# Optimization experiments

Measured on AMD Instinct MI355X. Metric: run time of the kernel, lower is better.

The kernel has to match this reference:

```python
import jax, jax.numpy as jnp
import numpy as np

B, L, E, H, C, V = 2048, 64, 200, 128, 128, 50000
EPS = 1e-5

def _gru_dir(x, Wih, Whh, bih, bhh):
    # x: [B, L, E] -> [B, L, H]; torch GRU gate order (r, z, n)
    xp = jnp.einsum('ble,ge->blg', x, Wih) + bih  # [B, L, 3H]
    xp = jnp.transpose(xp, (1, 0, 2))             # [L, B, 3H]
    h0 = jnp.zeros((x.shape[0], Whh.shape[1]), x.dtype)
    def step(h, xt):
        hp = h @ Whh.T + bhh
        xr, xz, xn = jnp.split(xt, 3, axis=-1)
        hr, hz, hn = jnp.split(hp, 3, axis=-1)
        r = jax.nn.sigmoid(xr + hr)
        z = jax.nn.sigmoid(xz + hz)
        n = jnp.tanh(xn + r * hn)
        h_new = (1.0 - z) * n + z * h
        return h_new, h_new
    _, ys = jax.lax.scan(step, h0, xp)
    return jnp.transpose(ys, (1, 0, 2))

def setup_inputs():
    key = jax.random.key(0)
    ks = jax.random.split(key, 16)
    sh = 1.0 / float(np.sqrt(H))
    sp = 1.0 / float(np.sqrt(2 * H))
    u = lambda k, s, a: jax.random.uniform(k, s, jnp.float32, -a, a)
    return {
        'x': jax.random.randint(ks[0], (B, L), 0, V),
        'word_hidden_stat': jnp.zeros((2, B, H), jnp.float32),
        'sequence_lens': jax.random.randint(ks[1], (B,), 1, L + 1),
        'emb': jax.random.normal(ks[2], (V, E), jnp.float32),
        'Wih_f': u(ks[3], (3 * H, E), sh), 'Whh_f': u(ks[4], (3 * H, H), sh),
        'bih_f': u(ks[5], (3 * H,), sh), 'bhh_f': u(ks[6], (3 * H,), sh),
        'Wih_b': u(ks[7], (3 * H, E), sh), 'Whh_b': u(ks[8], (3 * H, H), sh),
        'bih_b': u(ks[9], (3 * H,), sh), 'bhh_b': u(ks[10], (3 * H,), sh),
        'Wp': u(ks[11], (C, 2 * H), sp), 'bp': u(ks[12], (C,), sp),
        'gamma': jnp.ones((L,), jnp.float32), 'beta': jnp.zeros((L,), jnp.float32),
        'ctx': jax.random.uniform(ks[13], (C,), jnp.float32, -0.1, 0.1),
    }

def reference(x, word_hidden_stat, sequence_lens, emb, Wih_f, Whh_f, bih_f, bhh_f,
              Wih_b, Whh_b, bih_b, bhh_b, Wp, bp, gamma, beta, ctx):
    we = emb[x]                                            # [B, L, E]
    out_f = _gru_dir(we, Wih_f, Whh_f, bih_f, bhh_f)
    out_b = _gru_dir(we[:, ::-1], Wih_b, Whh_b, bih_b, bhh_b)[:, ::-1]
    out = jnp.concatenate([out_f, out_b], axis=-1)          # [B, L, 2H]
    # vectorized equivalent of get_mask + _fetch: zero positions >= length
    mask = (jnp.arange(L)[None, :] < sequence_lens[:, None]).astype(out.dtype)
    out = out * mask[:, :, None]
    proj = jnp.einsum('bld,cd->blc', out, Wp) + bp          # [B, L, C]
    # BatchNorm1d(num_features=L) in training mode: normalize each seq position over (batch, C)
    mean = proj.mean(axis=(0, 2), keepdims=True)
    var = proj.var(axis=(0, 2), keepdims=True)
    proj = (proj - mean) * jax.lax.rsqrt(var + EPS)
    proj = proj * gamma[None, :, None] + beta[None, :, None]
    proj = jax.nn.relu(proj)
    att = jax.nn.softmax(proj @ ctx, axis=1)                # [B, L]
    return jnp.einsum('bld,bl->bd', out, att)               # [B, 2H]
```

## Files before the change

### kernel.cpp

```cpp
#include <hip/hip_runtime.h>
#include <math.h>

#define BB 2048
#define LL 64
#define EE 200
#define HH 128
#define CDIM 128
#define VV 50000
#define G3 384
#define PEW 768
#define D2H 256
#define EPSV 1e-5f

typedef __attribute__((ext_vector_type(8))) short short8v;
typedef __attribute__((ext_vector_type(4))) float f32x4;

__device__ __forceinline__ float fast_sigmoid(float v) {
    return __builtin_amdgcn_rcpf(1.f + __expf(-v));
}
__device__ __forceinline__ float fast_tanh(float a) {
    float e = __expf(-2.f * fabsf(a));
    float m = (1.f - e) * __builtin_amdgcn_rcpf(1.f + e);
    return copysignf(m, a);
}

__device__ __forceinline__ float bf2f(unsigned short u) {
    union { unsigned int i; float f; } c; c.i = ((unsigned int)u) << 16; return c.f;
}
__device__ __forceinline__ unsigned short f2bf(float f) {
    union { float f; unsigned int i; } c; c.f = f;
    unsigned int r = c.i + 0x7FFF + ((c.i >> 16) & 1);
    return (unsigned short)(r >> 16);
}
__device__ __forceinline__ float ldc(const float* p) { return *p; }
__device__ __forceinline__ float ldc(const unsigned short* p) { return bf2f(*p); }
__device__ __forceinline__ void stc(float* p, float v) { *p = v; }
__device__ __forceinline__ void stc(unsigned short* p, float v) { *p = f2bf(v); }
__device__ __forceinline__ float4 ld4(const float* p) { return *(const float4*)p; }
__device__ __forceinline__ float4 ld4(const unsigned short* p) {
    ushort4 u = *(const ushort4*)p;
    return make_float4(bf2f(u.x), bf2f(u.y), bf2f(u.z), bf2f(u.w));
}

__global__ void zero_stats_kernel(float* __restrict__ stats) {
    if (threadIdx.x < 2 * LL) stats[threadIdx.x] = 0.f;
}

template <typename T>
__global__ __launch_bounds__(256) void pe_kernel(
    const float* __restrict__ emb,
    const float* __restrict__ Wih_f, const float* __restrict__ bih_f,
    const float* __restrict__ Wih_b, const float* __restrict__ bih_b,
    T* __restrict__ PE)
{
    __shared__ float As[8][136];
    __shared__ float Bs[8][136];
    const int mb = blockIdx.x * 128;
    const int nb = blockIdx.y * 128;
    const float* W  = (nb < G3) ? Wih_f : Wih_b;
    const float* bi = (nb < G3) ? bih_f : bih_b;
    const int nloc  = (nb < G3) ? nb : nb - G3;
    const int t  = threadIdx.x;
    const int tr = t >> 4, tc = t & 15;
    const int r  = t >> 1, q = t & 1;
    float acc[8][8] = {};
    for (int k0 = 0; k0 < EE; k0 += 8) {
        float4 av, bv;
        const int arow = mb + r;
        if (arow < VV) av = *(const float4*)(emb + (size_t)arow * EE + k0 + q * 4);
        else           av = make_float4(0.f, 0.f, 0.f, 0.f);
        bv = *(const float4*)(W + (size_t)(nloc + r) * EE + k0 + q * 4);
        __syncthreads();
        #pragma unroll
        for (int m = 0; m < 4; ++m) {
            As[q * 4 + m][r] = (&av.x)[m];
            Bs[q * 4 + m][r] = (&bv.x)[m];
        }
        __syncthreads();
        #pragma unroll
        for (int k = 0; k < 8; ++k) {
            float4 a0 = *(const float4*)&As[k][tr * 4];
            float4 a1 = *(const float4*)&As[k][64 + tr * 4];
            float4 b0 = *(const float4*)&Bs[k][tc * 4];
            float4 b1 = *(const float4*)&Bs[k][64 + tc * 4];
            float a8[8] = {a0.x,a0.y,a0.z,a0.w,a1.x,a1.y,a1.z,a1.w};
            float b8[8] = {b0.x,b0.y,b0.z,b0.w,b1.x,b1.y,b1.z,b1.w};
            #pragma unroll
            for (int i = 0; i < 8; ++i)
                #pragma unroll
                for (int j = 0; j < 8; ++j)
                    acc[i][j] = fmaf(a8[i], b8[j], acc[i][j]);
        }
    }
    #pragma unroll
    for (int i = 0; i < 8; ++i) {
        const int rl  = (i < 4) ? (tr * 4 + i) : (64 + tr * 4 + i - 4);
        const int row = mb + rl;
        if (row >= VV) continue;
        #pragma unroll
        for (int j = 0; j < 8; ++j) {
            const int cl = (j < 4) ? (tc * 4 + j) : (64 + tc * 4 + j - 4);
            stc(&PE[(size_t)row * PEW + nb + cl], acc[i][j] + bi[nloc + cl]);
        }
    }
}

__global__ void transpose4_kernel(const float* __restrict__ src,
                                  float* __restrict__ dst, int R, int K) {
    int idx = blockIdx.x * blockDim.x + threadIdx.x;
    int total = R * (K >> 2);
    if (idx >= total) return;
    int k4 = idx / R, r = idx - k4 * R;
    float4 v;
    v.x = src[r * K + k4 * 4 + 0];
    v.y = src[r * K + k4 * 4 + 1];
    v.z = src[r * K + k4 * 4 + 2];
    v.w = src[r * K + k4 * 4 + 3];
    ((float4*)dst)[idx] = v;
}

__global__ __launch_bounds__(64) void pack_whh_kernel(
    const float* __restrict__ Whh_f, const float* __restrict__ Whh_b,
    unsigned short* __restrict__ Wpk)
{
    const int fid = blockIdx.x;
    const int l   = threadIdx.x;
    const int g   = fid % 3;
    const int kt  = (fid / 3) & 3;
    const int p   = (fid / 12) & 1;
    const int w   = (fid / 24) & 7;
    const int dir = fid / 192;
    const float* W = dir ? Whh_b : Whh_f;
    const int n  = g * HH + w * 16 + (l & 15);
    const int k0 = kt * 32 + (l >> 4) * 8;
    unsigned short* dst = Wpk + (size_t)fid * 512 + l * 8;
    #pragma unroll
    for (int r = 0; r < 8; ++r) {
        float v = W[(size_t)n * HH + k0 + r];
        unsigned short hi = f2bf(v);
        dst[r] = p ? f2bf(v - bf2f(hi)) : hi;
    }
}

__global__ __launch_bounds__(64) void pack_wp_kernel(
    const float* __restrict__ Wp, unsigned short* __restrict__ WpPk)
{
    const int fid = blockIdx.x;
    const int l   = threadIdx.x;
    const int nt  = fid & 7;
    const int kt  = (fid >> 3) & 7;
    const int p   = fid >> 6;
    const int n   = nt * 16 + (l & 15);
    const int k0  = kt * 32 + (l >> 4) * 8;
    unsigned short* dst = WpPk + (size_t)fid * 512 + l * 8;
    #pragma unroll
    for (int r = 0; r < 8; ++r) {
        float v = Wp[(size_t)n * D2H + k0 + r];
        unsigned short hi = f2bf(v);
        dst[r] = p ? f2bf(v - bf2f(hi)) : hi;
    }
}

__global__ __launch_bounds__(64) void pack_wih_kernel(
    const float* __restrict__ Wih_f, const float* __restrict__ Wih_b,
    unsigned short* __restrict__ WihPk)
{
    const int fid = blockIdx.x;
    const int l   = threadIdx.x;
    const int nt  = fid % 48;
    const int kt  = (fid / 48) % 7;
    const int p   = fid / 336;
    const int n   = nt * 16 + (l & 15);
    const int k0  = kt * 32 + (l >> 4) * 8;
    const float* W = (n < G3) ? Wih_f : Wih_b;
    const int nl   = (n < G3) ? n : n - G3;
    unsigned short* dst = WihPk + (size_t)fid * 512 + l * 8;
    #pragma unroll
    for (int r = 0; r < 8; ++r) {
        const int k = k0 + r;
        float v = (k < EE) ? W[(size_t)nl * EE + k] : 0.f;
        unsigned short hi = f2bf(v);
        dst[r] = p ? f2bf(v - bf2f(hi)) : hi;
    }
}

__global__ __launch_bounds__(512) void pe_mfma_kernel(
    const float* __restrict__ emb,
    const unsigned short* __restrict__ WihPk,
    const float* __restrict__ bih_f, const float* __restrict__ bih_b,
    unsigned short* __restrict__ PE)
{
    __shared__ unsigned short ahi[64][264];
    const int b0 = blockIdx.x * 64;
    const int t  = threadIdx.x;
    const int w  = t >> 6, ln = t & 63;
    for (int idx = t; idx < 64 * 56; idx += 512) {
        const int r = idx / 56, q = idx - r * 56;
        const int row = b0 + r;
        float4 v = make_float4(0.f, 0.f, 0.f, 0.f);
        if (row < VV && q < 50)
            v = *(const float4*)(emb + (size_t)row * EE + q * 4);
        ushort4 h4;
        #pragma unroll
        for (int m = 0; m < 4; ++m)
            (&h4.x)[m] = f2bf((&v.x)[m]);
        *(ushort4*)&ahi[r][q * 4] = h4;
    }
    __syncthreads();
    const int sa = ln & 15, ka = (ln >> 4) * 8;
    const int rb = (ln >> 4) * 4;
    #pragma unroll
    for (int it = 0; it < 3; ++it) {
        const int ntb = it * 16 + w * 2;
        f32x4 acc[4][2];
        #pragma unroll
        for (int mt = 0; mt < 4; ++mt)
            #pragma unroll
            for (int n2 = 0; n2 < 2; ++n2)
                acc[mt][n2] = (f32x4){0.f, 0.f, 0.f, 0.f};
        #pragma unroll
        for (int kt = 0; kt < 7; ++kt) {
            short8v ah[4];
            #pragma unroll
            for (int mt = 0; mt < 4; ++mt)
                ah[mt] = *(const short8v*)&ahi[mt * 16 + sa][kt * 32 + ka];
            const unsigned short* bb = WihPk + ((size_t)(kt * 48 + ntb)) * 512 + (size_t)ln * 8;
            short8v bh0 = *(const short8v*)(bb);
            short8v bh1 = *(const short8v*)(bb + 512);
            short8v bl0 = *(const short8v*)(bb + (size_t)336 * 512);
            short8v bl1 = *(const short8v*)(bb + (size_t)336 * 512 + 512);
            #pragma unroll
            for (int mt = 0; mt < 4; ++mt) {
                acc[mt][0] = __builtin_amdgcn_mfma_f32_16x16x32_bf16(ah[mt], bh0, acc[mt][0], 0, 0, 0);
                acc[mt][0] = __builtin_amdgcn_mfma_f32_16x16x32_bf16(ah[mt], bl0, acc[mt][0], 0, 0, 0);
                acc[mt][1] = __builtin_amdgcn_mfma_f32_16x16x32_bf16(ah[mt], bh1, acc[mt][1], 0, 0, 0);
                acc[mt][1] = __builtin_amdgcn_mfma_f32_16x16x32_bf16(ah[mt], bl1, acc[mt][1], 0, 0, 0);
            }
        }
        #pragma unroll
        for (int n2 = 0; n2 < 2; ++n2) {
            const int col = (ntb + n2) * 16 + (ln & 15);
            const float bias = (col < G3) ? bih_f[col] : bih_b[col - G3];
            #pragma unroll
            for (int mt = 0; mt < 4; ++mt) {
                #pragma unroll
                for (int reg = 0; reg < 4; ++reg) {
                    const int row = b0 + mt * 16 + rb + reg;
                    if (row < VV)
                        stc(&PE[(size_t)row * PEW + col], acc[mt][n2][reg] + bias);
                }
            }
        }
    }
}

template <typename TPE, typename TOUT>
__global__ __launch_bounds__(512, 2) void gru_kernel(
    const int* __restrict__ xw, const int* __restrict__ lens,
    const TPE* __restrict__ PE,
    const unsigned short* __restrict__ Wpk,
    const float* __restrict__ bhh_f, const float* __restrict__ bhh_b,
    TOUT* __restrict__ out)
{
    const int dir = blockIdx.x >> 7;
    const int b0  = (blockIdx.x & 127) * 16;
    const float* bhh = dir ? bhh_b : bhh_f;
    const int t = threadIdx.x;
    const int w = t >> 6;
    const int l = t & 63;
    const int j  = w * 16 + (l & 15);
    const int sb = (l >> 4) * 4;
    const int sa = l & 15;
    const int ka = (l >> 4) * 8;
    __shared__ unsigned short hh[2][16][136];

    short8v wb[4][3];
    #pragma unroll
    for (int kt = 0; kt < 4; ++kt)
        #pragma unroll
        for (int g = 0; g < 3; ++g) {
            const size_t fid = (size_t)(dir * 192 + w * 24 + kt * 3 + g);
            wb[kt][g] = *(const short8v*)(Wpk + fid * 512 + (size_t)l * 8);
        }
    for (int i = t; i < 16 * 136; i += 512)
        ((unsigned short*)hh[0])[i] = 0;
    const float br  = bhh[j], bz = bhh[HH + j], bn_ = bhh[2 * HH + j];
    int lens_r[4];
    #pragma unroll
    for (int r = 0; r < 4; ++r) lens_r[r] = lens[b0 + sb + r];
    const int peBase = dir * G3;
    float hprev[4] = {0.f, 0.f, 0.f, 0.f};
    float xr[4], xz[4], xn[4];
    {
        const int lseq = dir ? (LL - 1) : 0;
        #pragma unroll
        for (int r = 0; r < 4; ++r) {
            const int tok = xw[(b0 + sb + r) * LL + lseq];
            const TPE* pp = PE + (size_t)tok * PEW + peBase + j;
            xr[r] = ldc(pp); xz[r] = ldc(pp + HH); xn[r] = ldc(pp + 2 * HH);
        }
    }
    __syncthreads();

    for (int step = 0; step < LL; ++step) {
        const int cur = step & 1, nxt = cur ^ 1;
        const int lseq = dir ? (LL - 1 - step) : step;
        short8v ah[4];
        #pragma unroll
        for (int kt = 0; kt < 4; ++kt)
            ah[kt] = *(const short8v*)&hh[cur][sa][kt * 32 + ka];
        float xrn[4], xzn[4], xnn[4];
        {
            int lq = dir ? (LL - 2 - step) : (step + 1);
            lq = lq < 0 ? 0 : (lq > LL - 1 ? LL - 1 : lq);
            #pragma unroll
            for (int r = 0; r < 4; ++r) {
                const int tok = xw[(b0 + sb + r) * LL + lq];
                const TPE* pp = PE + (size_t)tok * PEW + peBase + j;
                xrn[r] = ldc(pp); xzn[r] = ldc(pp + HH); xnn[r] = ldc(pp + 2 * HH);
            }
        }
        f32x4 aR = {0.f,0.f,0.f,0.f}, aZ = {0.f,0.f,0.f,0.f}, aN = {0.f,0.f,0.f,0.f};
        #pragma unroll
        for (int kt = 0; kt < 4; ++kt) {
            aR = __builtin_amdgcn_mfma_f32_16x16x32_bf16(ah[kt], wb[kt][0], aR, 0, 0, 0);
            aZ = __builtin_amdgcn_mfma_f32_16x16x32_bf16(ah[kt], wb[kt][1], aZ, 0, 0, 0);
            aN = __builtin_amdgcn_mfma_f32_16x16x32_bf16(ah[kt], wb[kt][2], aN, 0, 0, 0);
        }
        #pragma unroll
        for (int r = 0; r < 4; ++r) {
            const int s = sb + r;
            const float rr = fast_sigmoid(xr[r] + aR[r] + br);
            const float zz = fast_sigmoid(xz[r] + aZ[r] + bz);
            const float nn = fast_tanh(xn[r] + rr * (aN[r] + bn_));
            const float h  = (1.f - zz) * nn + zz * hprev[r];
            hprev[r] = h;
            hh[nxt][s][j] = f2bf(h);
            stc(&out[((size_t)(b0 + s) * LL + lseq) * D2H + dir * HH + j],
                (lseq < lens_r[r]) ? h : 0.f);
        }
        #pragma unroll
        for (int r = 0; r < 4; ++r) {
            xr[r] = xrn[r]; xz[r] = xzn[r]; xn[r] = xnn[r];
        }
        __builtin_amdgcn_sched_barrier(0);
        asm volatile("s_waitcnt lgkmcnt(0)" ::: "memory");
        __builtin_amdgcn_s_barrier();
        __builtin_amdgcn_sched_barrier(0);
    }
}

template <typename TOUT>
__global__ __launch_bounds__(256) void proj_kernel(
    const TOUT* __restrict__ out, const float* __restrict__ WpT4,
    const float* __restrict__ bp,
    float* __restrict__ proj, float* __restrict__ stats)
{
    __shared__ float outs[32][D2H];
    __shared__ float red[2][4];
    const int b0 = blockIdx.x * 32;
    const int l  = blockIdx.y;
    const int t  = threadIdx.x;
    for (int idx = t; idx < 32 * (D2H / 4); idx += 256) {
        int r = idx >> 6, c4 = idx & 63;
        float4 v = ld4(out + ((size_t)(b0 + r) * LL + l) * D2H + c4 * 4);
        *((float4*)&outs[r][c4 * 4]) = v;
    }
    __syncthreads();
    const int tr = t >> 5;
    const int tc = t & 31;
    float acc[4][4] = {};
    for (int k4 = 0; k4 < D2H / 4; ++k4) {
        float4 w[4];
        #pragma unroll
        for (int jj = 0; jj < 4; ++jj)
            w[jj] = ((const float4*)WpT4)[k4 * CDIM + tc * 4 + jj];
        #pragma unroll
        for (int i = 0; i < 4; ++i) {
            float4 a = *((const float4*)&outs[tr * 4 + i][k4 * 4]);
            #pragma unroll
            for (int jj = 0; jj < 4; ++jj) {
                acc[i][jj] = fmaf(a.x, w[jj].x, acc[i][jj]);
                acc[i][jj] = fmaf(a.y, w[jj].y, acc[i][jj]);
                acc[i][jj] = fmaf(a.z, w[jj].z, acc[i][jj]);
                acc[i][jj] = fmaf(a.w, w[jj].w, acc[i][jj]);
            }
        }
    }
    float s1 = 0.f, s2 = 0.f;
    #pragma unroll
    for (int i = 0; i < 4; ++i) {
        int b = b0 + tr * 4 + i;
        float4 pv;
        #pragma unroll
        for (int jj = 0; jj < 4; ++jj) {
            float v = acc[i][jj] + bp[tc * 4 + jj];
            (&pv.x)[jj] = v;
            s1 += v; s2 += v * v;
        }
        *((float4*)(proj + ((size_t)b * LL + l) * CDIM + tc * 4)) = pv;
    }
    #pragma unroll
    for (int off = 32; off > 0; off >>= 1) {
        s1 += __shfl_down(s1, off);
        s2 += __shfl_down(s2, off);
    }
    const int lane = t & 63, wv = t >> 6;
    if (lane == 0) { red[0][wv] = s1; red[1][wv] = s2; }
    __syncthreads();
    if (t == 0) {
        atomicAdd(&stats[l],      red[0][0] + red[0][1] + red[0][2] + red[0][3]);
        atomicAdd(&stats[LL + l], red[1][0] + red[1][1] + red[1][2] + red[1][3]);
    }
}

__global__ __launch_bounds__(512) void proj_mfma_kernel(
    const unsigned short* __restrict__ out, const unsigned short* __restrict__ WpPk,
    const float* __restrict__ bp,
    float* __restrict__ proj, float* __restrict__ stats)
{
    __shared__ unsigned short outs[64][264];
    __shared__ float red[2][8];
    const int b0 = blockIdx.x * 64;
    const int l  = blockIdx.y;
    const int t  = threadIdx.x;
    const int w  = t >> 6, ln = t & 63;
    for (int idx = t; idx < 64 * 32; idx += 512) {
        const int r = idx >> 5, c8 = idx & 31;
        *(short8v*)&outs[r][c8 * 8] =
            *(const short8v*)(out + ((size_t)(b0 + r) * LL + l) * D2H + c8 * 8);
    }
    __syncthreads();
    const int sa = ln & 15, ka = (ln >> 4) * 8;
    f32x4 acc[4];
    #pragma unroll
    for (int mt = 0; mt < 4; ++mt) acc[mt] = (f32x4){0.f, 0.f, 0.f, 0.f};
    #pragma unroll
    for (int kt = 0; kt < 8; ++kt) {
        short8v a[4];
        #pragma unroll
        for (int mt = 0; mt < 4; ++mt)
            a[mt] = *(const short8v*)&outs[mt * 16 + sa][kt * 32 + ka];
        const unsigned short* bbase = WpPk + ((size_t)kt * 8 + w) * 512 + (size_t)ln * 8;
        short8v bh = *(const short8v*)(bbase);
        short8v bl = *(const short8v*)(bbase + 64 * 512);
        #pragma unroll
        for (int mt = 0; mt < 4; ++mt) {
            acc[mt] = __builtin_amdgcn_mfma_f32_16x16x32_bf16(a[mt], bh, acc[mt], 0, 0, 0);
            acc[mt] = __builtin_amdgcn_mfma_f32_16x16x32_bf16(a[mt], bl, acc[mt], 0, 0, 0);
        }
    }
    float s1 = 0.f, s2 = 0.f;
    const int rb = (ln >> 4) * 4;
    const int col = w * 16 + (ln & 15);
    const float bpv = bp[col];
    #pragma unroll
    for (int mt = 0; mt < 4; ++mt) {
        #pragma unroll
        for (int reg = 0; reg < 4; ++reg) {
            const int row = b0 + mt * 16 + rb + reg;
            const float v = acc[mt][reg] + bpv;
            proj[((size_t)row * LL + l) * CDIM + col] = v;
            s1 += v; s2 += v * v;
        }
    }
    #pragma unroll
    for (int off = 32; off > 0; off >>= 1) {
        s1 += __shfl_down(s1, off);
        s2 += __shfl_down(s2, off);
    }
    if (ln == 0) { red[0][w] = s1; red[1][w] = s2; }
    __syncthreads();
    if (t == 0) {
        float r1 = 0.f, r2 = 0.f;
        #pragma unroll
        for (int i = 0; i < 8; ++i) { r1 += red[0][i]; r2 += red[1][i]; }
        atomicAdd(&stats[l], r1);
        atomicAdd(&stats[LL + l], r2);
    }
}

__global__ __launch_bounds__(256) void logits_kernel(
    const float* __restrict__ proj, const float* __restrict__ stats,
    const float* __restrict__ gamma, const float* __restrict__ beta,
    const float* __restrict__ ctx, float* __restrict__ logits)
{
    const int idx  = blockIdx.x * 4 + (threadIdx.x >> 6);
    const int lane = threadIdx.x & 63;
    const int b = idx >> 6, l = idx & 63;
    const float invN = 1.f / (float)(BB * CDIM);
    const float mean = stats[l] * invN;
    const float var  = stats[LL + l] * invN - mean * mean;
    const float inv  = rsqrtf(var + EPSV);
    const float g = gamma[l], be = beta[l];
    const float2 p = ((const float2*)(proj + ((size_t)b * LL + l) * CDIM))[lane];
    const float2 c = ((const float2*)ctx)[lane];
    float v0 = fmaxf((p.x - mean) * inv * g + be, 0.f);
    float v1 = fmaxf((p.y - mean) * inv * g + be, 0.f);
    float s = v0 * c.x + v1 * c.y;
    #pragma unroll
    for (int off = 32; off > 0; off >>= 1) s += __shfl_down(s, off);
    if (lane == 0) logits[idx] = s;
}

template <typename TOUT>
__global__ __launch_bounds__(256) void att_out_kernel(
    const TOUT* __restrict__ out, const float* __restrict__ logits,
    float* __restrict__ y)
{
    const int b = blockIdx.x;
    const int t = threadIdx.x;
    __shared__ float att[LL];
    if (t < 64) {
        float v = logits[b * LL + t];
        float m = v;
        #pragma unroll
        for (int off = 32; off > 0; off >>= 1) m = fmaxf(m, __shfl_xor(m, off));
        float e = __expf(v - m);
        float ssum = e;
        #pragma unroll
        for (int off = 32; off > 0; off >>= 1) ssum += __shfl_xor(ssum, off);
        att[t] = e / ssum;
    }
    __syncthreads();
    float acc = 0.f;
    const TOUT* ob = out + (size_t)b * LL * D2H + t;
    #pragma unroll
    for (int l = 0; l < LL; ++l) acc = fmaf(ldc(ob + (size_t)l * D2H), att[l], acc);
    y[b * D2H + t] = acc;
}

extern "C" void kernel_launch(void* const* d_in, const int* in_sizes, int n_in,
                              void* d_out, int out_size, void* d_ws, size_t ws_size,
                              hipStream_t stream) {
    const int*   xw     = (const int*)d_in[0];
    const int*   lens   = (const int*)d_in[2];
    const float* emb    = (const float*)d_in[3];
    const float* Wih_f  = (const float*)d_in[4];
    const float* Whh_f  = (const float*)d_in[5];
    const float* bih_f  = (const float*)d_in[6];
    const float* bhh_f  = (const float*)d_in[7];
    const float* Wih_b  = (const float*)d_in[8];
    const float* Whh_b  = (const float*)d_in[9];
    const float* bih_b  = (const float*)d_in[10];
    const float* bhh_b  = (const float*)d_in[11];
    const float* Wp     = (const float*)d_in[12];
    const float* bp     = (const float*)d_in[13];
    const float* gamma  = (const float*)d_in[14];
    const float* beta   = (const float*)d_in[15];
    const float* ctx    = (const float*)d_in[16];
    float* y = (float*)d_out;

    char* base = (char*)d_ws;
    size_t off = 0;
    auto alloc = [&](size_t bytes) -> void* {
        void* p = base + off; off += (bytes + 255) & ~(size_t)255; return p;
    };
    float* WpT4  = (float*)alloc((size_t)CDIM * D2H * 4);
    float* stats = (float*)alloc(2 * LL * 4);
    float* logit = (float*)alloc((size_t)BB * LL * 4);
    unsigned short* Wpk   = (unsigned short*)alloc((size_t)384 * 512 * 2);
    unsigned short* WpPk  = (unsigned short*)alloc((size_t)128 * 512 * 2);
    unsigned short* WihPk = (unsigned short*)alloc((size_t)672 * 512 * 2);
    const size_t extras = off;
    const size_t peB_A  = (size_t)VV * PEW * 4;
    const size_t outB_A = (size_t)BB * LL * D2H * 4;
    const size_t needA  = extras + peB_A + outB_A + 4096;
    const bool planA = ws_size >= needA;

    zero_stats_kernel<<<1, 128, 0, stream>>>(stats);
    pack_whh_kernel<<<384, 64, 0, stream>>>(Whh_f, Whh_b, Wpk);

    if (planA) {
        transpose4_kernel<<<(CDIM * D2H / 4 + 255) / 256, 256, 0, stream>>>(Wp, WpT4, CDIM, D2H);
        float* PE   = (float*)alloc(peB_A);
        float* outb = (float*)alloc(outB_A);
        float* proj = (float*)PE;
        pe_kernel<float><<<dim3((VV + 127) / 128, PEW / 128), 256, 0, stream>>>(
            emb, Wih_f, bih_f, Wih_b, bih_b, PE);
        gru_kernel<float, float><<<256, 512, 0, stream>>>(
            xw, lens, PE, Wpk, bhh_f, bhh_b, outb);
        proj_kernel<float><<<dim3(BB / 32, LL), 256, 0, stream>>>(outb, WpT4, bp, proj, stats);
        logits_kernel<<<BB * LL / 4, 256, 0, stream>>>(proj, stats, gamma, beta, ctx, logit);
        att_out_kernel<float><<<BB, 256, 0, stream>>>(outb, logit, y);
    } else {
        pack_wp_kernel<<<128, 64, 0, stream>>>(Wp, WpPk);
        pack_wih_kernel<<<672, 64, 0, stream>>>(Wih_f, Wih_b, WihPk);
        unsigned short* PE   = (unsigned short*)alloc((size_t)VV * PEW * 2);
        unsigned short* outb = (unsigned short*)alloc((size_t)BB * LL * D2H * 2);
        float* proj = (float*)PE;
        pe_mfma_kernel<<<(VV + 63) / 64, 512, 0, stream>>>(
            emb, WihPk, bih_f, bih_b, PE);
        gru_kernel<unsigned short, unsigned short><<<256, 512, 0, stream>>>(
            xw, lens, PE, Wpk, bhh_f, bhh_b, outb);
        proj_mfma_kernel<<<dim3(BB / 64, LL), 512, 0, stream>>>(outb, WpPk, bp, proj, stats);
        logits_kernel<<<BB * LL / 4, 256, 0, stream>>>(proj, stats, gamma, beta, ctx, logit);
        att_out_kernel<unsigned short><<<BB, 256, 0, stream>>>(outb, logit, y);
    }
}
```

Measured before the change: 212.5 us.

## Drop bf16 lo-split weight passes, enlarge PE tile, cache tokens in LDS

Removes the second MFMA pass that used the low-order bf16 residual of the weights in both the input-projection (PE) and output-projection kernels, halving their matrix work at the cost of weight precision. The PE kernel now processes 128 vocabulary rows per block instead of 64 and loads A fragments inside the inner loop. The GRU kernel stages each block's token ids in shared memory so per-step global index loads are avoided. It also writes the already rounded bf16 hidden value directly to the output instead of converting again. Reduced precision may push results past the tolerance, and the larger tile raises register pressure.

```diff
diff --git a/kernel.cpp b/kernel.cpp
--- a/kernel.cpp
+++ b/kernel.cpp
@@ -190,11 +190,11 @@
     const float* __restrict__ bih_f, const float* __restrict__ bih_b,
     unsigned short* __restrict__ PE)
 {
-    __shared__ unsigned short ahi[64][264];
-    const int b0 = blockIdx.x * 64;
+    __shared__ unsigned short ahi[128][264];
+    const int b0 = blockIdx.x * 128;
     const int t  = threadIdx.x;
     const int w  = t >> 6, ln = t & 63;
-    for (int idx = t; idx < 64 * 56; idx += 512) {
+    for (int idx = t; idx < 128 * 56; idx += 512) {
         const int r = idx / 56, q = idx - r * 56;
         const int row = b0 + r;
         float4 v = make_float4(0.f, 0.f, 0.f, 0.f);
@@ -209,32 +209,24 @@
     __syncthreads();
     const int sa = ln & 15, ka = (ln >> 4) * 8;
     const int rb = (ln >> 4) * 4;
-    #pragma unroll
     for (int it = 0; it < 3; ++it) {
         const int ntb = it * 16 + w * 2;
-        f32x4 acc[4][2];
-        #pragma unroll
-        for (int mt = 0; mt < 4; ++mt)
+        f32x4 acc[8][2];
+        #pragma unroll
+        for (int mt = 0; mt < 8; ++mt)
             #pragma unroll
             for (int n2 = 0; n2 < 2; ++n2)
                 acc[mt][n2] = (f32x4){0.f, 0.f, 0.f, 0.f};
         #pragma unroll
         for (int kt = 0; kt < 7; ++kt) {
-            short8v ah[4];
-            #pragma unroll
-            for (int mt = 0; mt < 4; ++mt)
-                ah[mt] = *(const short8v*)&ahi[mt * 16 + sa][kt * 32 + ka];
             const unsigned short* bb = WihPk + ((size_t)(kt * 48 + ntb)) * 512 + (size_t)ln * 8;
             short8v bh0 = *(const short8v*)(bb);
             short8v bh1 = *(const short8v*)(bb + 512);
-            short8v bl0 = *(const short8v*)(bb + (size_t)336 * 512);
-            short8v bl1 = *(const short8v*)(bb + (size_t)336 * 512 + 512);
             #pragma unroll
-            for (int mt = 0; mt < 4; ++mt) {
-                acc[mt][0] = __builtin_amdgcn_mfma_f32_16x16x32_bf16(ah[mt], bh0, acc[mt][0], 0, 0, 0);
-                acc[mt][0] = __builtin_amdgcn_mfma_f32_16x16x32_bf16(ah[mt], bl0, acc[mt][0], 0, 0, 0);
-                acc[mt][1] = __builtin_amdgcn_mfma_f32_16x16x32_bf16(ah[mt], bh1, acc[mt][1], 0, 0, 0);
-                acc[mt][1] = __builtin_amdgcn_mfma_f32_16x16x32_bf16(ah[mt], bl1, acc[mt][1], 0, 0, 0);
+            for (int mt = 0; mt < 8; ++mt) {
+                short8v ah = *(const short8v*)&ahi[mt * 16 + sa][kt * 32 + ka];
+                acc[mt][0] = __builtin_amdgcn_mfma_f32_16x16x32_bf16(ah, bh0, acc[mt][0], 0, 0, 0);
+                acc[mt][1] = __builtin_amdgcn_mfma_f32_16x16x32_bf16(ah, bh1, acc[mt][1], 0, 0, 0);
             }
         }
         #pragma unroll
@@ -242,7 +234,7 @@
             const int col = (ntb + n2) * 16 + (ln & 15);
             const float bias = (col < G3) ? bih_f[col] : bih_b[col - G3];
             #pragma unroll
-            for (int mt = 0; mt < 4; ++mt) {
+            for (int mt = 0; mt < 8; ++mt) {
                 #pragma unroll
                 for (int reg = 0; reg < 4; ++reg) {
                     const int row = b0 + mt * 16 + rb + reg;
@@ -273,6 +265,7 @@
     const int sa = l & 15;
     const int ka = (l >> 4) * 8;
     __shared__ unsigned short hh[2][16][136];
+    __shared__ int toks[16][LL];
 
     short8v wb[4][3];
     #pragma unroll
@@ -284,23 +277,24 @@
         }
     for (int i = t; i < 16 * 136; i += 512)
         ((unsigned short*)hh[0])[i] = 0;
+    for (int i = t; i < 16 * LL; i += 512)
+        ((int*)toks)[i] = xw[b0 * LL + i];
     const float br  = bhh[j], bz = bhh[HH + j], bn_ = bhh[2 * HH + j];
     int lens_r[4];
     #pragma unroll
     for (int r = 0; r < 4; ++r) lens_r[r] = lens[b0 + sb + r];
     const int peBase = dir * G3;
     float hprev[4] = {0.f, 0.f, 0.f, 0.f};
+    __syncthreads();
     float xr[4], xz[4], xn[4];
     {
         const int lseq = dir ? (LL - 1) : 0;
         #pragma unroll
         for (int r = 0; r < 4; ++r) {
-            const int tok = xw[(b0 + sb + r) * LL + lseq];
-            const TPE* pp = PE + (size_t)tok * PEW + peBase + j;
+            const TPE* pp = PE + (size_t)toks[sb + r][lseq] * PEW + peBase + j;
             xr[r] = ldc(pp); xz[r] = ldc(pp + HH); xn[r] = ldc(pp + 2 * HH);
         }
     }
-    __syncthreads();
 
     for (int step = 0; step < LL; ++step) {
         const int cur = step & 1, nxt = cur ^ 1;
@@ -315,8 +309,7 @@
             lq = lq < 0 ? 0 : (lq > LL - 1 ? LL - 1 : lq);
             #pragma unroll
             for (int r = 0; r < 4; ++r) {
-                const int tok = xw[(b0 + sb + r) * LL + lq];
-                const TPE* pp = PE + (size_t)tok * PEW + peBase + j;
+                const TPE* pp = PE + (size_t)toks[sb + r][lq] * PEW + peBase + j;
                 xrn[r] = ldc(pp); xzn[r] = ldc(pp + HH); xnn[r] = ldc(pp + 2 * HH);
             }
         }
@@ -335,9 +328,14 @@
             const float nn = fast_tanh(xn[r] + rr * (aN[r] + bn_));
             const float h  = (1.f - zz) * nn + zz * hprev[r];
             hprev[r] = h;
-            hh[nxt][s][j] = f2bf(h);
-            stc(&out[((size_t)(b0 + s) * LL + lseq) * D2H + dir * HH + j],
-                (lseq < lens_r[r]) ? h : 0.f);
+            const unsigned short us = f2bf(h);
+            hh[nxt][s][j] = us;
+            TOUT* po = &out[((size_t)(b0 + s) * LL + lseq) * D2H + dir * HH + j];
+            if constexpr (sizeof(TOUT) == 2) {
+                *(unsigned short*)po = (lseq < lens_r[r]) ? us : (unsigned short)0;
+            } else {
+                stc(po, (lseq < lens_r[r]) ? h : 0.f);
+            }
         }
         #pragma unroll
         for (int r = 0; r < 4; ++r) {
@@ -443,12 +441,9 @@
             a[mt] = *(const short8v*)&outs[mt * 16 + sa][kt * 32 + ka];
         const unsigned short* bbase = WpPk + ((size_t)kt * 8 + w) * 512 + (size_t)ln * 8;
         short8v bh = *(const short8v*)(bbase);
-        short8v bl = *(const short8v*)(bbase + 64 * 512);
-        #pragma unroll
-        for (int mt = 0; mt < 4; ++mt) {
+        #pragma unroll
+        for (int mt = 0; mt < 4; ++mt)
             acc[mt] = __builtin_amdgcn_mfma_f32_16x16x32_bf16(a[mt], bh, acc[mt], 0, 0, 0);
-            acc[mt] = __builtin_amdgcn_mfma_f32_16x16x32_bf16(a[mt], bl, acc[mt], 0, 0, 0);
-        }
     }
     float s1 = 0.f, s2 = 0.f;
     const int rb = (ln >> 4) * 4;
@@ -589,7 +584,7 @@
         unsigned short* PE   = (unsigned short*)alloc((size_t)VV * PEW * 2);
         unsigned short* outb = (unsigned short*)alloc((size_t)BB * LL * D2H * 2);
         float* proj = (float*)PE;
-        pe_mfma_kernel<<<(VV + 63) / 64, 512, 0, stream>>>(
+        pe_mfma_kernel<<<(VV + 127) / 128, 512, 0, stream>>>(
             emb, WihPk, bih_f, bih_b, PE);
         gru_kernel<unsigned short, unsigned short><<<256, 512, 0, stream>>>(
             xw, lens, PE, Wpk, bhh_f, bhh_b, outb);
```

After: 276.1 us. 29.9% more time.
